# Performance work log

Measured on AMD Instinct MI355X. Metric: run time of the kernel, lower is better.

## Reference

```python
import jax, jax.numpy as jnp
import numpy as np


def setup_inputs() -> dict:
    key = jax.random.key(0)
    k1, k2 = jax.random.split(key)
    B, T, K, D = 8, 4096, 1024, 256
    x = jax.random.normal(k1, (B, T, D), dtype=jnp.float32)
    codebook = jax.random.normal(k2, (K, D), dtype=jnp.float32)
    return {"x": x, "codebook": codebook}


def reference(x, codebook):
    # Faithful to: dist = tf.norm(z_e - lookup_, axis=-1); argmin(dist, -1).
    # argmin of the Euclidean norm == argmin of the squared distance, so we
    # instead of materializing the (B, T, k, d) broadcast intermediate.
    x2 = jnp.sum(x * x, axis=-1, keepdims=True)          # (B, T, 1)
    c2 = jnp.sum(codebook * codebook, axis=-1)           # (k,)
    xc = jnp.einsum('btd,kd->btk', x, codebook)          # (B, T, k)
    dist2 = x2 + c2 - 2.0 * xc                           # (B, T, k)
    return jnp.argmin(dist2, axis=-1)                    # (B, T) int
```

## Files before the change

kernel.cpp:

```cpp
#include <hip/hip_runtime.h>
#include <stdint.h>

typedef __attribute__((ext_vector_type(8))) _Float16 f16x8;
typedef __attribute__((ext_vector_type(4))) float f32x4;

#define MARG 0.09375f

__device__ __forceinline__ void glds16(const void* g, void* l) {
  __builtin_amdgcn_global_load_lds(
      (const __attribute__((address_space(1))) void*)g,
      (__attribute__((address_space(3))) void*)l, 16, 0, 0);
}

__device__ __forceinline__ unsigned short f2h(float f) {
  return __builtin_bit_cast(unsigned short, (_Float16)f);
}

__global__ __launch_bounds__(256) void vq_prep_cb(const float* __restrict__ cb,
                                                  unsigned short* __restrict__ cbh,
                                                  float* __restrict__ hc,
                                                  int* __restrict__ count) {
  int w = threadIdx.x >> 6, lane = threadIdx.x & 63;
  int row = blockIdx.x * 4 + w;
  size_t off = (size_t)row * 256 + lane * 4;
  float4 v = *reinterpret_cast<const float4*>(cb + off);
  ushort4 h;
  h.x = f2h(v.x); h.y = f2h(v.y); h.z = f2h(v.z); h.w = f2h(v.w);
  *reinterpret_cast<ushort4*>(cbh + off) = h;
  float s = v.x * v.x + v.y * v.y + v.z * v.z + v.w * v.w;
#pragma unroll
  for (int m = 32; m >= 1; m >>= 1) s += __shfl_xor(s, m, 64);
  if (lane == 0) hc[row] = 0.5f * s;
  if (blockIdx.x == 0 && threadIdx.x == 0) *count = 0;
}

__global__ __launch_bounds__(512, 2) void vq_mfma_kernel(
    const float* __restrict__ x, const unsigned short* __restrict__ cbh,
    const float* __restrict__ hc, int* __restrict__ out,
    int* __restrict__ list, int* __restrict__ count) {
  __shared__ unsigned short Alds[16384];
  __shared__ unsigned short Blds[32768];
  __shared__ float c2s[1024];
  __shared__ float cbv[4][64];
  __shared__ int   cbi[4][64];
  __shared__ float csv[4][64];

  const int tid = threadIdx.x;
  const int lane = tid & 63;
  const int wave = tid >> 6;
  const int wr = wave >> 2;
  const int wc = wave & 3;
  const int l15 = lane & 15;
  const int l4  = lane >> 4;
  const int bswz = (blockIdx.x & 7) * 64 + (blockIdx.x >> 3);
  const int r0 = bswz * 64;

  auto stage = [&](int T1) {
    const int p = T1 & 1;
    const int n0 = (T1 >> 2) << 8;
    const int d0 = (T1 & 3) << 6;
    unsigned short* B = Blds + p * 16384;
#pragma unroll
    for (int r = 0; r < 4; ++r) {
      int idx = r * 512 + tid;
      int code = idx >> 3;
      int lc = (idx & 7) ^ (code & 7);
      glds16(cbh + (size_t)(n0 + code) * 256 + d0 + lc * 8, B + idx * 8);
    }
  };

  stage(0);

  reinterpret_cast<float2*>(c2s)[tid] = reinterpret_cast<const float2*>(hc)[tid];

  {
    const int row = tid >> 3;
    const int cc  = tid & 7;
    const float* src = x + (size_t)(r0 + row) * 256 + cc * 32;
    unsigned short hv[32];
#pragma unroll
    for (int q = 0; q < 8; ++q) {
      float4 v = *reinterpret_cast<const float4*>(src + q * 4);
      hv[q * 4 + 0] = f2h(v.x); hv[q * 4 + 1] = f2h(v.y);
      hv[q * 4 + 2] = f2h(v.z); hv[q * 4 + 3] = f2h(v.w);
    }
    char* base = reinterpret_cast<char*>(Alds);
#pragma unroll
    for (int g = 0; g < 4; ++g) {
      int byte = (row * 512 + cc * 64 + g * 16) ^ ((row & 7) << 4);
      *reinterpret_cast<f16x8*>(base + byte) = *reinterpret_cast<const f16x8*>(&hv[g * 8]);
    }
  }
  __syncthreads();

  f16x8 af[2][8];
  {
    const char* Ab = reinterpret_cast<const char*>(Alds);
#pragma unroll
    for (int tr = 0; tr < 2; ++tr) {
      int arow = wr * 32 + tr * 16 + l15;
      int abase = (arow * 512 + l4 * 16) ^ ((arow & 7) << 4);
#pragma unroll
      for (int dt = 0; dt < 8; ++dt)
        af[tr][dt] = *reinterpret_cast<const f16x8*>(Ab + (abase ^ (dt * 64)));
    }
  }

  float bestv[2][4], secondv[2][4];
  int besti[2][4];
#pragma unroll
  for (int tr = 0; tr < 2; ++tr)
#pragma unroll
    for (int g = 0; g < 4; ++g) {
      bestv[tr][g] = -3.4e38f; secondv[tr][g] = -3.4e38f; besti[tr][g] = 0;
    }

  const int bcol0 = wc * 64;

#pragma unroll
  for (int nt = 0; nt < 4; ++nt) {
    f32x4 acc[2][4];
#pragma unroll
    for (int tr = 0; tr < 2; ++tr)
#pragma unroll
      for (int tc = 0; tc < 4; ++tc) acc[tr][tc] = (f32x4){0.f, 0.f, 0.f, 0.f};

#pragma unroll
    for (int s = 0; s < 4; ++s) {
      const int T = nt * 4 + s;
      const int p = T & 1;
      if (T < 15) {
        stage(T + 1);
        asm volatile("s_waitcnt vmcnt(4)" ::: "memory");
      } else {
        asm volatile("s_waitcnt vmcnt(0)" ::: "memory");
      }
      __builtin_amdgcn_s_barrier();

      const unsigned short* B = Blds + p * 16384;
#pragma unroll
      for (int kk = 0; kk < 2; ++kk) {
        f16x8 bf[4];
#pragma unroll
        for (int tc = 0; tc < 4; ++tc) {
          int bcol = bcol0 + tc * 16 + l15;
          int g = kk * 4 + l4;
          bf[tc] = *reinterpret_cast<const f16x8*>(B + bcol * 64 + ((g ^ (bcol & 7)) * 8));
        }
#pragma unroll
        for (int tr = 0; tr < 2; ++tr)
#pragma unroll
          for (int tc = 0; tc < 4; ++tc)
            acc[tr][tc] = __builtin_amdgcn_mfma_f32_16x16x32_f16(
                af[tr][s * 2 + kk], bf[tc], acc[tr][tc], 0, 0, 0);
      }

      asm volatile("s_waitcnt lgkmcnt(0)" ::: "memory");
      __builtin_amdgcn_s_barrier();
    }

    const int cb0 = nt * 256 + bcol0 + l15;
    float hcv[4];
#pragma unroll
    for (int tc = 0; tc < 4; ++tc) hcv[tc] = c2s[cb0 + tc * 16];
#pragma unroll
    for (int tr = 0; tr < 2; ++tr)
#pragma unroll
      for (int tc = 0; tc < 4; ++tc) {
        const int code = cb0 + tc * 16;
#pragma unroll
        for (int g = 0; g < 4; ++g) {
          float s = acc[tr][tc][g] - hcv[tc];
          bool gt = s > bestv[tr][g];
          float ns = gt ? bestv[tr][g] : fmaxf(secondv[tr][g], s);
          bestv[tr][g] = gt ? s : bestv[tr][g];
          besti[tr][g] = gt ? code : besti[tr][g];
          secondv[tr][g] = ns;
        }
      }
  }

#pragma unroll
  for (int tr = 0; tr < 2; ++tr)
#pragma unroll
    for (int g = 0; g < 4; ++g) {
      float bv = bestv[tr][g]; int bi = besti[tr][g]; float sv = secondv[tr][g];
#pragma unroll
      for (int m = 1; m < 16; m <<= 1) {
        float ov = __shfl_xor(bv, m, 64);
        int   oi = __shfl_xor(bi, m, 64);
        float os = __shfl_xor(sv, m, 64);
        sv = fmaxf(fmaxf(sv, os), fminf(bv, ov));
        bool gt = (ov > bv) || (ov == bv && oi < bi);
        bv = gt ? ov : bv;
        bi = gt ? oi : bi;
      }
      if (l15 == 0) {
        int rl = wr * 32 + tr * 16 + l4 * 4 + g;
        cbv[wc][rl] = bv; cbi[wc][rl] = bi; csv[wc][rl] = sv;
      }
    }

  __syncthreads();
  if (tid < 64) {
    float bv = cbv[0][tid]; int bi = cbi[0][tid]; float sv = csv[0][tid];
#pragma unroll
    for (int w2 = 1; w2 < 4; ++w2) {
      float ov = cbv[w2][tid]; int oi = cbi[w2][tid]; float os = csv[w2][tid];
      sv = fmaxf(fmaxf(sv, os), fminf(bv, ov));
      bool gt = (ov > bv) || (ov == bv && oi < bi);
      bv = gt ? ov : bv;
      bi = gt ? oi : bi;
    }
    out[r0 + tid] = bi;
    if (sv >= bv - MARG) {
      int slot = atomicAdd(count, 1);
      list[slot] = r0 + tid;
    }
  }
}

__global__ __launch_bounds__(512) void vq_cleanup(const float* __restrict__ x,
                                                  const float* __restrict__ cb,
                                                  const float* __restrict__ hc,
                                                  const int* __restrict__ list,
                                                  const int* __restrict__ count,
                                                  int* __restrict__ out) {
  __shared__ float xt[8][256];
  __shared__ int rowids[8];
  __shared__ float wbv[8][8];
  __shared__ int   wbi[8][8];
  const int tid = threadIdx.x;
  const int wave = tid >> 6;
  const int n = *count;

  for (int t0 = blockIdx.x * 8; t0 < n; t0 += gridDim.x * 8) {
    __syncthreads();
    if (tid < 8) rowids[tid] = (t0 + tid < n) ? list[t0 + tid] : -1;
    __syncthreads();
    {
      int j = tid >> 6, seg = tid & 63;
      int row = rowids[j];
      if (row < 0) row = rowids[0];
      *reinterpret_cast<float4*>(&xt[j][seg * 4]) =
          *reinterpret_cast<const float4*>(x + (size_t)row * 256 + seg * 4);
    }
    __syncthreads();

    float acc0[8], acc1[8];
#pragma unroll
    for (int j = 0; j < 8; ++j) { acc0[j] = 0.f; acc1[j] = 0.f; }

    const float* c0 = cb + (size_t)tid * 256;
    const float* c1 = cb + (size_t)(512 + tid) * 256;
#pragma unroll 4
    for (int d0 = 0; d0 < 256; d0 += 4) {
      float4 ca = *reinterpret_cast<const float4*>(c0 + d0);
      float4 cd = *reinterpret_cast<const float4*>(c1 + d0);
#pragma unroll
      for (int j = 0; j < 8; ++j) {
        float4 xv = *reinterpret_cast<const float4*>(&xt[j][d0]);
        acc0[j] = fmaf(ca.x, xv.x, acc0[j]);
        acc0[j] = fmaf(ca.y, xv.y, acc0[j]);
        acc0[j] = fmaf(ca.z, xv.z, acc0[j]);
        acc0[j] = fmaf(ca.w, xv.w, acc0[j]);
        acc1[j] = fmaf(cd.x, xv.x, acc1[j]);
        acc1[j] = fmaf(cd.y, xv.y, acc1[j]);
        acc1[j] = fmaf(cd.z, xv.z, acc1[j]);
        acc1[j] = fmaf(cd.w, xv.w, acc1[j]);
      }
    }

    const float h0 = hc[tid];
    const float h1 = hc[512 + tid];

#pragma unroll
    for (int j = 0; j < 8; ++j) {
      float bv = acc0[j] - h0; int bi = tid;
      float s1 = acc1[j] - h1;
      if (s1 > bv) { bv = s1; bi = 512 + tid; }
#pragma unroll
      for (int m = 1; m < 64; m <<= 1) {
        float ov = __shfl_xor(bv, m, 64);
        int   oi = __shfl_xor(bi, m, 64);
        bool gt = (ov > bv) || (ov == bv && oi < bi);
        bv = gt ? ov : bv;
        bi = gt ? oi : bi;
      }
      if ((tid & 63) == 0) { wbv[wave][j] = bv; wbi[wave][j] = bi; }
    }
    __syncthreads();
    if (tid < 8 && rowids[tid] >= 0) {
      float bv = wbv[0][tid]; int bi = wbi[0][tid];
#pragma unroll
      for (int w2 = 1; w2 < 8; ++w2) {
        float ov = wbv[w2][tid]; int oi = wbi[w2][tid];
        if (ov > bv || (ov == bv && oi < bi)) { bv = ov; bi = oi; }
      }
      out[rowids[tid]] = bi;
    }
  }
}

#define BM 128
#define BN 256
#define BD 32
#define NT 512

__global__ __launch_bounds__(256) void vq_c2_kernel(const float* __restrict__ cb,
                                                    float* __restrict__ halfc2) {
  int row  = blockIdx.x * 4 + (threadIdx.x >> 6);
  int lane = threadIdx.x & 63;
  float4 v = *reinterpret_cast<const float4*>(cb + (size_t)row * 256 + lane * 4);
  float s = v.x * v.x + v.y * v.y + v.z * v.z + v.w * v.w;
#pragma unroll
  for (int m = 32; m >= 1; m >>= 1) s += __shfl_xor(s, m, 64);
  if (lane == 0) halfc2[row] = 0.5f * s;
}

__global__ __launch_bounds__(NT, 2) void vq_argmin_kernel(
    const float* __restrict__ x, const float* __restrict__ cb,
    const float* __restrict__ halfc2, int* __restrict__ out) {
  __shared__ float lds[2][(BM + BN) * BD];
  __shared__ float c2s[1024];
  const int tid = threadIdx.x;
  const int w   = tid >> 6;
  const int tc  = tid & 31;
  const int tr  = tid >> 5;
  const int r0  = blockIdx.x * BM;
  reinterpret_cast<float2*>(c2s)[tid] = reinterpret_cast<const float2*>(halfc2)[tid];
  const int sA  = tr & 7;
  const int sB  = tc & 7;
  const int sAB = sA ^ sB;
  const int cho = (((tid & 7) ^ w)) * 4;
  const int sub = tid >> 3;
  float bestv[8]; int besti[8];
#pragma unroll
  for (int i = 0; i < 8; ++i) { bestv[i] = -3.4e38f; besti[i] = 0; }
  auto stage = [&](int n0, int d0, int p) {
    float* dst  = &lds[p][0];
    float* dstB = dst + BM * BD;
#pragma unroll
    for (int r = 0; r < 2; ++r) {
      int t2 = r * NT + tid;
      glds16(x + (size_t)(r0 + r * 64 + sub) * 256 + d0 + cho, dst + t2 * 4);
    }
#pragma unroll
    for (int r = 0; r < 4; ++r) {
      int t2 = r * NT + tid;
      glds16(cb + (size_t)(n0 + r * 64 + sub) * 256 + d0 + cho, dstB + t2 * 4);
    }
  };
  stage(0, 0, 0);
  int t = 0;
  for (int nt = 0; nt < 4; ++nt) {
    float acc[8][8];
#pragma unroll
    for (int i = 0; i < 8; ++i)
#pragma unroll
      for (int j = 0; j < 8; ++j) acc[i][j] = 0.f;
    for (int dt = 0; dt < 8; ++dt, ++t) {
      const int p = t & 1;
      if (t < 31) {
        const int t1 = t + 1;
        stage((t1 >> 3) * BN, (t1 & 7) * BD, t1 & 1);
        asm volatile("s_waitcnt vmcnt(6)" ::: "memory");
      } else {
        asm volatile("s_waitcnt vmcnt(0)" ::: "memory");
      }
      __builtin_amdgcn_s_barrier();
      const float* pA = &lds[p][tr * 8 * BD];
      const float* pB = &lds[p][BM * BD + tc * 8 * BD];
#pragma unroll
      for (int cc = 0; cc < 8; ++cc) {
        const float* pBc = pB + ((cc ^ sAB) << 2);
        float4 a[8], b[8];
#pragma unroll
        for (int i = 0; i < 8; ++i)
          a[i] = *reinterpret_cast<const float4*>(pA + i * BD + cc * 4);
#pragma unroll
        for (int j = 0; j < 8; ++j)
          b[j] = *reinterpret_cast<const float4*>(pBc + j * BD);
#pragma unroll
        for (int i = 0; i < 8; ++i)
#pragma unroll
          for (int j = 0; j < 8; ++j) {
            acc[i][j] = fmaf(a[i].x, b[j].x, acc[i][j]);
            acc[i][j] = fmaf(a[i].y, b[j].y, acc[i][j]);
            acc[i][j] = fmaf(a[i].z, b[j].z, acc[i][j]);
            acc[i][j] = fmaf(a[i].w, b[j].w, acc[i][j]);
          }
      }
      asm volatile("s_waitcnt lgkmcnt(0)" ::: "memory");
      __builtin_amdgcn_s_barrier();
    }
    const int n0 = nt * BN;
#pragma unroll
    for (int j = 0; j < 8; ++j) {
      const int code = n0 + tc * 8 + j;
      const float hc = c2s[code];
#pragma unroll
      for (int i = 0; i < 8; ++i) {
        float s = acc[i][j] - hc;
        if (s > bestv[i]) { bestv[i] = s; besti[i] = code; }
      }
    }
  }
#pragma unroll
  for (int i = 0; i < 8; ++i) {
#pragma unroll
    for (int m = 1; m <= 16; m <<= 1) {
      float ov = __shfl_xor(bestv[i], m, 64);
      int   oi = __shfl_xor(besti[i], m, 64);
      if (ov > bestv[i] || (ov == bestv[i] && oi < besti[i])) { bestv[i] = ov; besti[i] = oi; }
    }
  }
  if (tc == 0) {
#pragma unroll
    for (int i = 0; i < 8; ++i) out[r0 + tr * 8 + i] = besti[i];
  }
}

extern "C" void kernel_launch(void* const* d_in, const int* in_sizes, int n_in,
                              void* d_out, int out_size, void* d_ws, size_t ws_size,
                              hipStream_t stream) {
  const float* x  = (const float*)d_in[0];
  const float* cb = (const float*)d_in[1];
  int* out = (int*)d_out;

  const size_t OFF_CH = 0;
  const size_t OFF_HC = OFF_CH + (size_t)1024 * 256 * 2;
  const size_t OFF_LS = OFF_HC + (size_t)1024 * 4;
  const size_t OFF_CT = OFF_LS + (size_t)32768 * 4;
  const size_t NEED   = OFF_CT + 64;

  if (ws_size >= NEED) {
    unsigned short* cbh = (unsigned short*)((char*)d_ws + OFF_CH);
    float* hc  = (float*)((char*)d_ws + OFF_HC);
    int* list  = (int*)((char*)d_ws + OFF_LS);
    int* count = (int*)((char*)d_ws + OFF_CT);

    hipLaunchKernelGGL(vq_prep_cb, dim3(256), dim3(256), 0, stream, cb, cbh, hc, count);
    hipLaunchKernelGGL(vq_mfma_kernel, dim3(512), dim3(512), 0, stream,
                       x, cbh, hc, out, list, count);
    hipLaunchKernelGGL(vq_cleanup, dim3(512), dim3(512), 0, stream,
                       x, cb, hc, list, count, out);
  } else {
    float* c2 = (float*)d_ws;
    hipLaunchKernelGGL(vq_c2_kernel, dim3(256), dim3(256), 0, stream, cb, c2);
    hipLaunchKernelGGL(vq_argmin_kernel, dim3(32768 / BM), dim3(NT), 0, stream,
                       x, cb, c2, out);
  }
}
```

Baseline: 84.43 us.

## Triple-buffer codebook tiles with one barrier per step and smaller LDS for 4 blocks/CU

Restructures the MFMA argmin kernel. The wave tiling changes from 2x4 to 4x2, so each wave handles 16 rows and 64 codes per 128-code tile. The A staging buffer is aliased into the B buffers, and the double-buffered 256-code tiles become a triple-buffered ring of 128-code tiles with one barrier per step and two tiles prefetched ahead. This cuts LDS use so launch bounds can request 4 blocks per CU, and it adds s_setprio around the MFMA section. The aim is more occupancy and fewer barrier stalls, at the cost of less register reuse per wave (one A fragment row block instead of two) and more B fragment loads per MFMA.

```diff
diff --git a/kernel.cpp b/kernel.cpp
--- a/kernel.cpp
+++ b/kernel.cpp
@@ -34,42 +34,25 @@
   if (blockIdx.x == 0 && threadIdx.x == 0) *count = 0;
 }
 
-__global__ __launch_bounds__(512, 2) void vq_mfma_kernel(
+__global__ __launch_bounds__(512, 4) void vq_mfma_kernel(
     const float* __restrict__ x, const unsigned short* __restrict__ cbh,
     const float* __restrict__ hc, int* __restrict__ out,
     int* __restrict__ list, int* __restrict__ count) {
-  __shared__ unsigned short Alds[16384];
-  __shared__ unsigned short Blds[32768];
+  __shared__ unsigned short Blds[3 * 8192];
   __shared__ float c2s[1024];
-  __shared__ float cbv[4][64];
-  __shared__ int   cbi[4][64];
-  __shared__ float csv[4][64];
+  __shared__ float cbv[2][64];
+  __shared__ int   cbi[2][64];
+  __shared__ float csv[2][64];
 
   const int tid = threadIdx.x;
   const int lane = tid & 63;
   const int wave = tid >> 6;
-  const int wr = wave >> 2;
-  const int wc = wave & 3;
+  const int wr = wave >> 1;
+  const int wc = wave & 1;
   const int l15 = lane & 15;
   const int l4  = lane >> 4;
   const int bswz = (blockIdx.x & 7) * 64 + (blockIdx.x >> 3);
   const int r0 = bswz * 64;
-
-  auto stage = [&](int T1) {
-    const int p = T1 & 1;
-    const int n0 = (T1 >> 2) << 8;
-    const int d0 = (T1 & 3) << 6;
-    unsigned short* B = Blds + p * 16384;
-#pragma unroll
-    for (int r = 0; r < 4; ++r) {
-      int idx = r * 512 + tid;
-      int code = idx >> 3;
-      int lc = (idx & 7) ^ (code & 7);
-      glds16(cbh + (size_t)(n0 + code) * 256 + d0 + lc * 8, B + idx * 8);
-    }
-  };
-
-  stage(0);
 
   reinterpret_cast<float2*>(c2s)[tid] = reinterpret_cast<const float2*>(hc)[tid];
 
@@ -84,7 +67,7 @@
       hv[q * 4 + 0] = f2h(v.x); hv[q * 4 + 1] = f2h(v.y);
       hv[q * 4 + 2] = f2h(v.z); hv[q * 4 + 3] = f2h(v.w);
     }
-    char* base = reinterpret_cast<char*>(Alds);
+    char* base = reinterpret_cast<char*>(Blds);
 #pragma unroll
     for (int g = 0; g < 4; ++g) {
       int byte = (row * 512 + cc * 64 + g * 16) ^ ((row & 7) << 4);
@@ -93,125 +76,120 @@
   }
   __syncthreads();
 
-  f16x8 af[2][8];
+  f16x8 af[8];
   {
-    const char* Ab = reinterpret_cast<const char*>(Alds);
-#pragma unroll
-    for (int tr = 0; tr < 2; ++tr) {
-      int arow = wr * 32 + tr * 16 + l15;
-      int abase = (arow * 512 + l4 * 16) ^ ((arow & 7) << 4);
-#pragma unroll
-      for (int dt = 0; dt < 8; ++dt)
-        af[tr][dt] = *reinterpret_cast<const f16x8*>(Ab + (abase ^ (dt * 64)));
-    }
-  }
-
-  float bestv[2][4], secondv[2][4];
-  int besti[2][4];
-#pragma unroll
-  for (int tr = 0; tr < 2; ++tr)
-#pragma unroll
-    for (int g = 0; g < 4; ++g) {
-      bestv[tr][g] = -3.4e38f; secondv[tr][g] = -3.4e38f; besti[tr][g] = 0;
-    }
-
-  const int bcol0 = wc * 64;
-
-#pragma unroll
-  for (int nt = 0; nt < 4; ++nt) {
-    f32x4 acc[2][4];
-#pragma unroll
-    for (int tr = 0; tr < 2; ++tr)
-#pragma unroll
-      for (int tc = 0; tc < 4; ++tc) acc[tr][tc] = (f32x4){0.f, 0.f, 0.f, 0.f};
+    const char* Ab = reinterpret_cast<const char*>(Blds);
+    int arow = wr * 16 + l15;
+    int abase = (arow * 512 + l4 * 16) ^ ((arow & 7) << 4);
+#pragma unroll
+    for (int dt = 0; dt < 8; ++dt)
+      af[dt] = *reinterpret_cast<const f16x8*>(Ab + (abase ^ (dt * 64)));
+  }
+  __syncthreads();
+
+  auto stage = [&](int T1, int buf) {
+    const int n0 = (T1 >> 2) << 7;
+    const int d0 = (T1 & 3) << 6;
+    unsigned short* B = Blds + buf * 8192;
+#pragma unroll
+    for (int r = 0; r < 2; ++r) {
+      int idx = r * 512 + tid;
+      int c = idx >> 3;
+      int lg = (idx & 7) ^ (c & 7);
+      glds16(cbh + (size_t)(n0 + c) * 256 + d0 + lg * 8, B + idx * 8);
+    }
+  };
+
+  float bestv[4], secv[4];
+  int besti[4];
+#pragma unroll
+  for (int g = 0; g < 4; ++g) {
+    bestv[g] = -3.4e38f; secv[g] = -3.4e38f; besti[g] = 0;
+  }
+
+  stage(0, 0);
+  stage(1, 1);
+
+#pragma unroll
+  for (int nt = 0; nt < 8; ++nt) {
+    f32x4 acc[4];
+#pragma unroll
+    for (int tcx = 0; tcx < 4; ++tcx) acc[tcx] = (f32x4){0.f, 0.f, 0.f, 0.f};
 
 #pragma unroll
     for (int s = 0; s < 4; ++s) {
       const int T = nt * 4 + s;
-      const int p = T & 1;
-      if (T < 15) {
-        stage(T + 1);
-        asm volatile("s_waitcnt vmcnt(4)" ::: "memory");
+      if (T < 31) {
+        asm volatile("s_waitcnt vmcnt(2) lgkmcnt(0)" ::: "memory");
       } else {
-        asm volatile("s_waitcnt vmcnt(0)" ::: "memory");
-      }
-      __builtin_amdgcn_s_barrier();
-
-      const unsigned short* B = Blds + p * 16384;
+        asm volatile("s_waitcnt vmcnt(0) lgkmcnt(0)" ::: "memory");
+      }
+      asm volatile("s_barrier" ::: "memory");
+      if (T < 30) stage(T + 2, (T + 2) % 3);
+
+      const unsigned short* B = Blds + (T % 3) * 8192;
+      __builtin_amdgcn_s_setprio(1);
 #pragma unroll
       for (int kk = 0; kk < 2; ++kk) {
         f16x8 bf[4];
 #pragma unroll
-        for (int tc = 0; tc < 4; ++tc) {
-          int bcol = bcol0 + tc * 16 + l15;
-          int g = kk * 4 + l4;
-          bf[tc] = *reinterpret_cast<const f16x8*>(B + bcol * 64 + ((g ^ (bcol & 7)) * 8));
+        for (int tcx = 0; tcx < 4; ++tcx) {
+          int c = wc * 64 + tcx * 16 + l15;
+          int phys = (kk * 4 + l4) ^ (c & 7);
+          bf[tcx] = *reinterpret_cast<const f16x8*>(B + c * 64 + phys * 8);
         }
 #pragma unroll
-        for (int tr = 0; tr < 2; ++tr)
-#pragma unroll
-          for (int tc = 0; tc < 4; ++tc)
-            acc[tr][tc] = __builtin_amdgcn_mfma_f32_16x16x32_f16(
-                af[tr][s * 2 + kk], bf[tc], acc[tr][tc], 0, 0, 0);
-      }
-
-      asm volatile("s_waitcnt lgkmcnt(0)" ::: "memory");
-      __builtin_amdgcn_s_barrier();
-    }
-
-    const int cb0 = nt * 256 + bcol0 + l15;
-    float hcv[4];
-#pragma unroll
-    for (int tc = 0; tc < 4; ++tc) hcv[tc] = c2s[cb0 + tc * 16];
-#pragma unroll
-    for (int tr = 0; tr < 2; ++tr)
-#pragma unroll
-      for (int tc = 0; tc < 4; ++tc) {
-        const int code = cb0 + tc * 16;
-#pragma unroll
-        for (int g = 0; g < 4; ++g) {
-          float s = acc[tr][tc][g] - hcv[tc];
-          bool gt = s > bestv[tr][g];
-          float ns = gt ? bestv[tr][g] : fmaxf(secondv[tr][g], s);
-          bestv[tr][g] = gt ? s : bestv[tr][g];
-          besti[tr][g] = gt ? code : besti[tr][g];
-          secondv[tr][g] = ns;
-        }
-      }
-  }
-
-#pragma unroll
-  for (int tr = 0; tr < 2; ++tr)
-#pragma unroll
-    for (int g = 0; g < 4; ++g) {
-      float bv = bestv[tr][g]; int bi = besti[tr][g]; float sv = secondv[tr][g];
-#pragma unroll
-      for (int m = 1; m < 16; m <<= 1) {
-        float ov = __shfl_xor(bv, m, 64);
-        int   oi = __shfl_xor(bi, m, 64);
-        float os = __shfl_xor(sv, m, 64);
-        sv = fmaxf(fmaxf(sv, os), fminf(bv, ov));
-        bool gt = (ov > bv) || (ov == bv && oi < bi);
-        bv = gt ? ov : bv;
-        bi = gt ? oi : bi;
-      }
-      if (l15 == 0) {
-        int rl = wr * 32 + tr * 16 + l4 * 4 + g;
-        cbv[wc][rl] = bv; cbi[wc][rl] = bi; csv[wc][rl] = sv;
-      }
-    }
-
-  __syncthreads();
-  if (tid < 64) {
-    float bv = cbv[0][tid]; int bi = cbi[0][tid]; float sv = csv[0][tid];
-#pragma unroll
-    for (int w2 = 1; w2 < 4; ++w2) {
-      float ov = cbv[w2][tid]; int oi = cbi[w2][tid]; float os = csv[w2][tid];
+        for (int tcx = 0; tcx < 4; ++tcx)
+          acc[tcx] = __builtin_amdgcn_mfma_f32_16x16x32_f16(
+              af[s * 2 + kk], bf[tcx], acc[tcx], 0, 0, 0);
+      }
+      __builtin_amdgcn_s_setprio(0);
+    }
+
+    const int cb0 = nt * 128 + wc * 64 + l15;
+#pragma unroll
+    for (int tcx = 0; tcx < 4; ++tcx) {
+      const int code = cb0 + tcx * 16;
+      const float hcv = c2s[code];
+#pragma unroll
+      for (int g = 0; g < 4; ++g) {
+        float sc = acc[tcx][g] - hcv;
+        bool gt = sc > bestv[g];
+        float ns = gt ? bestv[g] : fmaxf(secv[g], sc);
+        bestv[g] = gt ? sc : bestv[g];
+        besti[g] = gt ? code : besti[g];
+        secv[g] = ns;
+      }
+    }
+  }
+
+#pragma unroll
+  for (int g = 0; g < 4; ++g) {
+    float bv = bestv[g]; int bi = besti[g]; float sv = secv[g];
+#pragma unroll
+    for (int m = 1; m < 16; m <<= 1) {
+      float ov = __shfl_xor(bv, m, 64);
+      int   oi = __shfl_xor(bi, m, 64);
+      float os = __shfl_xor(sv, m, 64);
       sv = fmaxf(fmaxf(sv, os), fminf(bv, ov));
       bool gt = (ov > bv) || (ov == bv && oi < bi);
       bv = gt ? ov : bv;
       bi = gt ? oi : bi;
     }
+    if (l15 == 0) {
+      int rl = wr * 16 + l4 * 4 + g;
+      cbv[wc][rl] = bv; cbi[wc][rl] = bi; csv[wc][rl] = sv;
+    }
+  }
+
+  __syncthreads();
+  if (tid < 64) {
+    float bv = cbv[0][tid]; int bi = cbi[0][tid]; float sv = csv[0][tid];
+    float ov = cbv[1][tid]; int oi = cbi[1][tid]; float os = csv[1][tid];
+    sv = fmaxf(fmaxf(sv, os), fminf(bv, ov));
+    bool gt = (ov > bv) || (ov == bv && oi < bi);
+    bv = gt ? ov : bv;
+    bi = gt ? oi : bi;
     out[r0 + tid] = bi;
     if (sv >= bv - MARG) {
       int slot = atomicAdd(count, 1);
```

Result: slower. 113.1 us (+34.0%).
